# Kernel optimization log

Measured on AMD Instinct MI355X. Metric: run time of the kernel, lower is better.

The kernel has to match this reference:

```python
import math
import jax, jax.numpy as jnp
import numpy as np

B, N, H, K = 8, 1024, 200, 3
EDGE_SIZE = 50

def _layernorm(x, g, b, eps=1e-20):
    mu = jnp.mean(x, -1, keepdims=True)
    var = jnp.mean((x - mu) ** 2, -1, keepdims=True)
    return (x - mu) / jnp.sqrt(var + eps) * g + b

def _bert_layer(x, mask_add, qw, qb, kw, kb, vw, vb, aow, aob, g1, b1, iw, ib, ow, ob, g2, b2):
    # single-head self-attention (num_heads=1 -> head_dim == H), eval mode (dropout = identity)
    q = x @ qw + qb
    k = x @ kw + kb
    v = x @ vw + vb
    scores = jnp.einsum('bnd,bmd->bnm', q, k) / math.sqrt(H) + mask_add  # [B,N,N]
    probs = jax.nn.softmax(scores, -1)
    ctx = jnp.einsum('bnm,bmd->bnd', probs, v)
    attn = _layernorm(ctx @ aow + aob + x, g1, b1)
    inter = jax.nn.gelu(attn @ iw + ib, approximate=False)
    return _layernorm(inter @ ow + ob + attn, g2, b2)

def setup_inputs():
    key = jax.random.key(0)
    ks = jax.random.split(key, 16)
    s = 0.02
    text = jax.random.normal(ks[0], (B, N, H), jnp.float32)
    adj1 = (jax.random.uniform(ks[1], (B, N, N)) < 0.02).astype(jnp.float32)
    adj1 = jnp.maximum(adj1, jnp.eye(N, dtype=jnp.float32))  # self loops
    adj2 = (jax.random.uniform(ks[2], (B, N, N)) < 0.02).astype(jnp.float32)
    edge1 = jax.random.randint(ks[3], (B, N, N), 0, EDGE_SIZE, jnp.int32)
    edge2 = jax.random.randint(ks[4], (B, N, N), 0, EDGE_SIZE, jnp.int32)
    lengths = jax.random.randint(ks[5], (B,), N // 2, N + 1)
    textmask = (jnp.arange(N)[None, :] < lengths[:, None]).astype(jnp.float32)
    def nrm(k, shape):
        return jax.random.normal(k, shape, jnp.float32) * s
    return dict(
        text=text, adj1=adj1, adj2=adj2, edge1=edge1, edge2=edge2, textmask=textmask,
        gcn_w=nrm(ks[6], (H, H)), mut_w=nrm(ks[7], (H, H)),
        qw=nrm(ks[8], (K, H, H)), qb=jnp.zeros((K, H), jnp.float32),
        kw=nrm(ks[9], (K, H, H)), kb=jnp.zeros((K, H), jnp.float32),
        vw=nrm(ks[10], (K, H, H)), vb=jnp.zeros((K, H), jnp.float32),
        aow=nrm(ks[11], (K, H, H)), aob=jnp.zeros((K, H), jnp.float32),
        ln1_g=jnp.ones((K, H), jnp.float32), ln1_b=jnp.zeros((K, H), jnp.float32),
        iw=nrm(ks[12], (K, H, H)), ib=jnp.zeros((K, H), jnp.float32),
        ow=nrm(ks[13], (K, H, H)), ob=jnp.zeros((K, H), jnp.float32),
        ln2_g=jnp.ones((K, H), jnp.float32), ln2_b=jnp.zeros((K, H), jnp.float32))

def reference(text, adj1, adj2, edge1, edge2, textmask, gcn_w, mut_w, qw, qb, kw, kb, vw, vb, aow, aob, ln1_g, ln1_b, iw, ib, ow, ob, ln2_g, ln2_b):
    # edge1/edge2 and edge_vocab are unused by the original forward
    adj = adj1 + adj2
    adj = jnp.where(adj >= 1.0, 1.0, adj)
    mask_add = ((1.0 - textmask) * -10000.0)[:, None, :]           # [B,1,N] key-side mask
    pair = textmask[:, :, None] * textmask[:, None, :]             # [B,N,N]
    pair_add = (1.0 - pair) * -10000.0
    denom = jnp.sum(adj, 2, keepdims=True) + 1e-07                 # [B,N,1]
    outs, output = text, text                                      # in_features == out_features path
    for i in range(K):
        outs = _bert_layer(outs, mask_add, qw[i], qb[i], kw[i], kb[i], vw[i], vb[i],
                           aow[i], aob[i], ln1_g[i], ln1_b[i], iw[i], ib[i], ow[i], ob[i], ln2_g[i], ln2_b[i])
        # GCN propagation: adj-matmul -> degree normalize -> relu -> residual (dropout = identity in eval)
        teout = output @ gcn_w
        output = jax.nn.relu(jnp.einsum('bnm,bmd->bnd', adj, teout) / denom) + output
        # selfalignment: dual masked softmax attention between outs and output
        logit = jnp.einsum('bnd,bmd->bnm', outs @ mut_w, output) + pair_add
        p_row = jax.nn.softmax(logit, -1)
        p_col = jax.nn.softmax(logit, -2)
        new_outs = jnp.einsum('bnm,bmd->bnd', p_row, output) * textmask[:, :, None] + outs
        output = jnp.einsum('bnm,bnd->bmd', p_col, outs) * textmask[:, :, None] + output
        outs = new_outs
    return outs, adj
```

## Files before the change

### kernel.cpp

```cpp
#include <hip/hip_runtime.h>
#include <hip/hip_bf16.h>
#include <math.h>

#define Bd 8
#define Nd 1024
#define Hd 200
#define HP 224
#define BN (Bd*Nd)
#define SZ_BNH ((size_t)BN*Hd)
#define SZ_BNN ((size_t)BN*Nd)
#define SZ_PAD ((size_t)BN*HP)

typedef __hip_bfloat16 bf16;
typedef __attribute__((ext_vector_type(8))) short bf16x8;
typedef __attribute__((ext_vector_type(4))) float f32x4;

__device__ __forceinline__ float bf2f(bf16 v){ return __bfloat162float(v); }
__device__ __forceinline__ bf16 f2bf(float v){ return __float2bfloat16(v); }

#define MFMA16(a,b,c) __builtin_amdgcn_mfma_f32_16x16x32_bf16((a),(b),(c),0,0,0)

__device__ __forceinline__ size_t tidx1024(int row, int k){
  return (size_t)(row>>4)*16384 + (size_t)((k>>5))*512
       + (size_t)(((k>>3)&3))*128 + (size_t)(row&15)*8 + (k&7);
}
__device__ __forceinline__ size_t tidxHP(int row, int k){
  return (size_t)(row>>4)*3584 + (size_t)((k>>5))*512
       + (size_t)(((k>>3)&3))*128 + (size_t)(row&15)*8 + (k&7);
}

__global__ void k_prep_masks(const float* __restrict__ tm, float* __restrict__ maskf,
                             float* __restrict__ maskadd){
  int i = blockIdx.x*256 + threadIdx.x;
  if (i < BN){ float m = tm[i]; maskf[i] = m; maskadd[i] = (1.f - m) * -10000.f; }
}

__global__ void k_prep_adj(const float* __restrict__ a1, const float* __restrict__ a2,
                           float* __restrict__ adj_out, float* __restrict__ denom){
  int r = blockIdx.x;
  const size_t base = (size_t)r * Nd;
  int t = threadIdx.x;
  float s = 0.f;
  for (int m = t; m < Nd; m += 256){
    float a = a1[base+m] + a2[base+m];
    a = a >= 1.f ? 1.f : a;
    adj_out[base+m] = a;
    s += a;
  }
  __shared__ float red[256];
  red[t] = s; __syncthreads();
  for (int st = 128; st > 0; st >>= 1){ if (t < st) red[t] += red[t+st]; __syncthreads(); }
  if (t == 0) denom[r] = red[0] + 1e-07f;
}

__global__ void k_copy2(const float* __restrict__ x, float* __restrict__ o1,
                        float* __restrict__ o2){
  size_t i = (size_t)blockIdx.x*256 + threadIdx.x;
  if (i < SZ_BNH){ float v = x[i]; o1[i] = v; o2[i] = v; }
}

__global__ void c_pad_split(const float* __restrict__ X, bf16* __restrict__ Oh,
                            bf16* __restrict__ Ol){
  size_t o = (size_t)blockIdx.x*256 + threadIdx.x;
  if (o >= SZ_PAD) return;
  int oi = (int)o;
  int panel = oi / 3584;
  int rem   = oi % 3584;
  int kt  = rem >> 9;
  int kg  = (rem >> 7) & 3;
  int r16 = (rem >> 3) & 15;
  int ke  = rem & 7;
  int row = panel*16 + r16;
  int k   = kt*32 + kg*8 + ke;
  float v = (k < Hd) ? X[(size_t)row*Hd + k] : 0.f;
  bf16 h = f2bf(v);
  Oh[o] = h; Ol[o] = f2bf(v - bf2f(h));
}

__global__ void c_padT_split(const float* __restrict__ X, bf16* __restrict__ Oh,
                             bf16* __restrict__ Ol){
  __shared__ float t[32][33];
  int b = blockIdx.z, m0 = blockIdx.x*32, d0 = blockIdx.y*32;
  int tx = threadIdx.x, ty = threadIdx.y;
  for (int i = ty; i < 32; i += 8){
    int d = d0 + tx;
    t[i][tx] = (d < Hd) ? X[((size_t)b*Nd + m0+i)*Hd + d] : 0.f;
  }
  __syncthreads();
  for (int i = ty; i < 32; i += 8){
    int row = d0 + i, kk = m0 + tx;
    size_t idx = (size_t)b*229376 + tidx1024(row, kk);
    float v = t[tx][i];
    bf16 h = f2bf(v);
    Oh[idx] = h; Ol[idx] = f2bf(v - bf2f(h));
  }
}

__global__ void c_w_split_all(const float* __restrict__ g, const float* __restrict__ m,
                              const float* __restrict__ q, const float* __restrict__ k,
                              const float* __restrict__ v, const float* __restrict__ ao,
                              const float* __restrict__ iw, const float* __restrict__ ow,
                              bf16* __restrict__ Oh, bf16* __restrict__ Ol){
  int mi = blockIdx.y;
  const float* W;
  if (mi == 0) W = g;
  else if (mi == 1) W = m;
  else {
    int gi = (mi-2)/3, si = (mi-2)%3;
    const float* bs[6] = {q, k, v, ao, iw, ow};
    W = bs[gi] + (size_t)si*Hd*Hd;
  }
  int o = blockIdx.x*256 + threadIdx.x;
  if (o >= HP*HP) return;
  int panel = o / 3584;
  int rem   = o % 3584;
  int kt  = rem >> 9;
  int kg  = (rem >> 7) & 3;
  int r16 = (rem >> 3) & 15;
  int ke  = rem & 7;
  int n   = panel*16 + r16;
  int kk  = kt*32 + kg*8 + ke;
  float val = (n < Hd && kk < Hd) ? W[kk*Hd + n] : 0.f;
  bf16 h = f2bf(val);
  Oh[(size_t)mi*HP*HP + o] = h; Ol[(size_t)mi*HP*HP + o] = f2bf(val - bf2f(h));
}

__global__ void c_cvt1024_t(const float* __restrict__ X, bf16* __restrict__ O){
  int b = blockIdx.z, kg = blockIdx.x, rg = blockIdx.y;
  int r = threadIdx.x >> 5, kl = threadIdx.x & 31;
  int row = rg*8 + r, k = kg*32 + kl;
  float v = X[(size_t)b*1048576 + (size_t)row*1024 + k];
  O[(size_t)b*1048576 + tidx1024(row, k)] = f2bf(v);
}

__global__ void c_pcolT_split(const float* __restrict__ S, const float* __restrict__ cmax,
                              const float* __restrict__ csum, bf16* __restrict__ Ph,
                              bf16* __restrict__ Pl){
  __shared__ float t[32][33];
  int b = blockIdx.z, n0 = blockIdx.x*32, m0 = blockIdx.y*32;
  int tx = threadIdx.x, ty = threadIdx.y;
  for (int i = ty; i < 32; i += 8)
    t[i][tx] = S[(size_t)b*Nd*Nd + (size_t)(n0+i)*Nd + m0 + tx];
  __syncthreads();
  for (int i = ty; i < 32; i += 8){
    int m = m0 + i;
    float cm = cmax[b*Nd + m], ci = 1.f / csum[b*Nd + m];
    float p = expf(t[tx][i] - cm) * ci;
    size_t idx = (size_t)b*1048576 + tidx1024(m, n0 + tx);
    bf16 h = f2bf(p);
    Ph[idx] = h; Pl[idx] = f2bf(p - bf2f(h));
  }
}

template<int SPLIT>
__global__ __launch_bounds__(256)
void k_rowsoftmax(const float* __restrict__ S, bf16* __restrict__ Ph,
                  bf16* __restrict__ Pl){
  __shared__ float row[Nd];
  __shared__ float red[256];
  size_t bid = blockIdx.x;
  size_t r = ((bid & 7) << 10) + (bid >> 3);
  const float* src = S + r*Nd;
  int t = threadIdx.x;
  float mx = -3.4e38f;
  for (int i = t; i < Nd; i += 256){ float v = src[i]; row[i] = v; mx = fmaxf(mx, v); }
  red[t] = mx; __syncthreads();
  for (int s = 128; s > 0; s >>= 1){ if (t < s) red[t] = fmaxf(red[t], red[t+s]); __syncthreads(); }
  mx = red[0]; __syncthreads();
  float sum = 0.f;
  for (int i = t; i < Nd; i += 256) sum += expf(row[i] - mx);
  red[t] = sum; __syncthreads();
  for (int s = 128; s > 0; s >>= 1){ if (t < s) red[t] += red[t+s]; __syncthreads(); }
  float inv = 1.f / red[0];
  size_t obase = ((r >> 10) << 20) + (size_t)(((int)(r & 1023)) >> 4)*16384
               + (size_t)((int)r & 15)*8;
  for (int i = t; i < Nd; i += 256){
    float p = expf(row[i] - mx) * inv;
    bf16 h = f2bf(p);
    size_t idx = obase + (size_t)(i>>5)*512 + (size_t)((i>>3)&3)*128 + (i&7);
    Ph[idx] = h;
    if (SPLIT) Pl[idx] = f2bf(p - bf2f(h));
  }
}

__global__ __launch_bounds__(1024)
void k_colstats(const float* __restrict__ S, float* __restrict__ cmax,
                float* __restrict__ csum){
  int b = blockIdx.y;
  int tx = threadIdx.x & 63, ty = threadIdx.x >> 6;
  int m = blockIdx.x*64 + tx;
  const float* Sbp = S + (size_t)b*Nd*Nd + m;
  float mx = -3.4e38f, sm = 0.f;
  for (int n = ty; n < Nd; n += 16){
    float x = Sbp[(size_t)n*Nd];
    if (x > mx){ sm = sm * expf(mx - x) + 1.f; mx = x; }
    else        sm += expf(x - mx);
  }
  __shared__ float smx[16][64], ssm[16][64];
  smx[ty][tx] = mx; ssm[ty][tx] = sm;
  __syncthreads();
  for (int st = 8; st > 0; st >>= 1){
    if (ty < st){
      float m1 = smx[ty][tx],    s1 = ssm[ty][tx];
      float m2 = smx[ty+st][tx], s2 = ssm[ty+st][tx];
      float M = fmaxf(m1, m2);
      smx[ty][tx] = M;
      ssm[ty][tx] = s1*expf(m1 - M) + s2*expf(m2 - M);
    }
    __syncthreads();
  }
  if (ty == 0){ cmax[b*Nd + m] = smx[0][tx]; csum[b*Nd + m] = ssm[0][tx]; }
}

__global__ void k_add_ln(const float* __restrict__ X, const float* __restrict__ R,
                         const float* __restrict__ g, const float* __restrict__ bb,
                         float* __restrict__ Y, bf16* __restrict__ Ph,
                         bf16* __restrict__ Pl){
  int r = blockIdx.x, t = threadIdx.x;
  __shared__ float red[256];
  bool act = t < Hd;
  float v = 0.f;
  if (act) v = X[(size_t)r*Hd + t] + R[(size_t)r*Hd + t];
  red[t] = act ? v : 0.f; __syncthreads();
  for (int s = 128; s > 0; s >>= 1){ if (t < s) red[t] += red[t+s]; __syncthreads(); }
  float mu = red[0] * (1.f/Hd); __syncthreads();
  float d = act ? (v - mu) : 0.f;
  red[t] = d*d; __syncthreads();
  for (int s = 128; s > 0; s >>= 1){ if (t < s) red[t] += red[t+s]; __syncthreads(); }
  float var = red[0] * (1.f/Hd);
  float o = 0.f;
  if (act){
    float rs = 1.f / sqrtf(var + 1e-20f);
    o = (v - mu) * rs * g[t] + bb[t];
    Y[(size_t)r*Hd + t] = o;
  }
  if (Ph && t < HP){
    bf16 h = f2bf(o);
    size_t idx = tidxHP(r, t);
    Ph[idx] = h; Pl[idx] = f2bf(o - bf2f(h));
  }
}

template<int EPI, int TERMS, int RI, int KP>
__global__ __launch_bounds__(256)
void k_mfma3(const bf16* __restrict__ Ah, const bf16* __restrict__ Al,
             const bf16* __restrict__ Bh, const bf16* __restrict__ Bl,
             float* __restrict__ Y, bf16* __restrict__ Ybh, bf16* __restrict__ Ybl,
             const float* __restrict__ bias, const float* __restrict__ e0,
             const float* __restrict__ e1,
             size_t sAb, size_t sBb, float scale)
{
  int b = blockIdx.z;
  int wave = threadIdx.x >> 6, lane = threadIdx.x & 63;
  int r0 = (blockIdx.y*4 + wave)*(RI*16);
  int c0 = blockIdx.x*64;
  int lm = lane & 15, lq = lane >> 4;
  const size_t PST = (size_t)16*KP;
  const size_t aT = (size_t)b*sAb + (size_t)(r0>>4)*PST + (size_t)lane*8;
  const size_t bT = (size_t)b*sBb + (size_t)(c0>>4)*PST + (size_t)lane*8;
  constexpr int STEPS = KP/32;

  f32x4 acc[RI][4] = {};
  bf16x8 pah[2][RI], pal[2][RI], pbh[2][4], pbl[2][4];
  {
    #pragma unroll
    for (int i = 0; i < RI; i++) pah[0][i] = *(const bf16x8*)(Ah + aT + (size_t)i*PST);
    #pragma unroll
    for (int j = 0; j < 4; j++){
      pbh[0][j] = *(const bf16x8*)(Bh + bT + (size_t)j*PST);
      pbl[0][j] = *(const bf16x8*)(Bl + bT + (size_t)j*PST);
    }
    if (TERMS >= 3){
      #pragma unroll
      for (int i = 0; i < RI; i++) pal[0][i] = *(const bf16x8*)(Al + aT + (size_t)i*PST);
    }
  }

  #pragma unroll
  for (int ki = 0; ki < STEPS; ki++){
    const int cb = ki & 1, nb = cb ^ 1;
    if (ki + 1 < STEPS){
      const size_t kn = (size_t)(ki+1)*512;
      #pragma unroll
      for (int i = 0; i < RI; i++) pah[nb][i] = *(const bf16x8*)(Ah + aT + (size_t)i*PST + kn);
      #pragma unroll
      for (int j = 0; j < 4; j++){
        pbh[nb][j] = *(const bf16x8*)(Bh + bT + (size_t)j*PST + kn);
        pbl[nb][j] = *(const bf16x8*)(Bl + bT + (size_t)j*PST + kn);
      }
      if (TERMS >= 3){
        #pragma unroll
        for (int i = 0; i < RI; i++) pal[nb][i] = *(const bf16x8*)(Al + aT + (size_t)i*PST + kn);
      }
    }
    #pragma unroll
    for (int i = 0; i < RI; i++)
      #pragma unroll
      for (int j = 0; j < 4; j++) acc[i][j] = MFMA16(pah[cb][i], pbh[cb][j], acc[i][j]);
    #pragma unroll
    for (int i = 0; i < RI; i++)
      #pragma unroll
      for (int j = 0; j < 4; j++) acc[i][j] = MFMA16(pah[cb][i], pbl[cb][j], acc[i][j]);
    if (TERMS >= 3){
      #pragma unroll
      for (int i = 0; i < RI; i++)
        #pragma unroll
        for (int j = 0; j < 4; j++) acc[i][j] = MFMA16(pal[cb][i], pbh[cb][j], acc[i][j]);
    }
  }

  if constexpr (EPI == 9){
    __shared__ float tl[64][65];
    #pragma unroll
    for (int j = 0; j < 4; j++)
      #pragma unroll
      for (int r = 0; r < 4; r++)
        tl[wave*16 + lq*4 + r][j*16 + lm] = acc[0][j][r];
    __syncthreads();
    int b2 = (int)((blockIdx.y*64) >> 10);
    int m0 = (int)((blockIdx.y*64) & 1023);
    #pragma unroll
    for (int e = threadIdx.x; e < 4096; e += 256){
      int pan = e >> 10, rem = e & 1023;
      int r16 = (rem >> 3) & 15;
      int d = c0 + pan*16 + r16;
      if (d >= HP) continue;
      int kg = (rem >> 7) & 3;
      int k_loc = (rem >> 9)*32 + kg*8 + (rem & 7);
      float val = 0.f;
      if (d < Hd) val = tl[k_loc][pan*16 + r16] + (bias ? bias[d] : 0.f);
      bf16 h = f2bf(val);
      size_t idx = (size_t)b2*229376 + (size_t)(d>>4)*16384
                 + (size_t)((m0 + k_loc)>>5)*512 + (size_t)kg*128
                 + (size_t)r16*8 + (rem & 7);
      Ybh[idx] = h; Ybl[idx] = f2bf(val - bf2f(h));
    }
  } else {
    #pragma unroll
    for (int i = 0; i < RI; i++){
      #pragma unroll
      for (int j = 0; j < 4; j++){
        int col = c0 + j*16 + lm;
        int rbase = r0 + i*16 + lq*4;
        #pragma unroll
        for (int r = 0; r < 4; r++){
          int row = rbase + r;
          size_t rowg = (size_t)b*Nd + row;
          float v = acc[i][j][r];
          if (EPI == 0){
            if (col < Hd){
              v += bias ? bias[col] : 0.f;
              Y[rowg*Hd + col] = v;
            }
          } else if (EPI == 2){
            if (col < HP){
              float o = (col < Hd) ? v + (bias ? bias[col] : 0.f) : 0.f;
              bf16 h = f2bf(o);
              size_t idx = tidxHP((int)rowg, col);
              Ybh[idx] = h;
              Ybl[idx] = f2bf(o - bf2f(h));
            }
          } else if (EPI == 3){
            Y[rowg*Nd + col] = v*scale + e0[b*Nd + col];
          } else if (EPI == 4){
            Y[rowg*Nd + col] = v + (1.f - e1[b*Nd+row]*e1[b*Nd+col])*(-10000.f);
          } else if (EPI == 10){
            if (col < HP){
              float o = 0.f;
              if (col < Hd){
                float vv = v + (bias ? bias[col] : 0.f);
                o = 0.5f*vv*(1.f + erff(vv*0.7071067811865476f));
              }
              bf16 h = f2bf(o);
              size_t idx = tidxHP((int)rowg, col);
              Ybh[idx] = h;
              Ybl[idx] = f2bf(o - bf2f(h));
            }
          }
        }
      }
    }
  }
}

template<int EPI, int TERMS, int KP>
__global__ __launch_bounds__(256)
void k_mfma3sk(const bf16* __restrict__ Ah, const bf16* __restrict__ Al,
               const bf16* __restrict__ Bh, const bf16* __restrict__ Bl,
               float* __restrict__ Y, bf16* __restrict__ Ybh, bf16* __restrict__ Ybl,
               const float* __restrict__ e0, const float* __restrict__ e1,
               const float* __restrict__ R,
               size_t sAb, size_t sBb)
{
  __shared__ float red[4][64][33];
  int b = blockIdx.z;
  int wave = threadIdx.x >> 6, lane = threadIdx.x & 63;
  int r0 = blockIdx.x*32;
  int c0 = blockIdx.y*64;
  int lm = lane & 15, lq = lane >> 4;
  const size_t aT = (size_t)b*sAb + (size_t)(r0>>4)*((size_t)16*KP) + (size_t)lane*8;
  const size_t bT = (size_t)b*sBb + (size_t)(c0>>4)*((size_t)16*KP) + (size_t)lane*8;
  const int kt0 = wave*(KP>>7);
  constexpr int STEPS = KP/128;

  f32x4 acc[2][4] = {};
  bf16x8 pah[2][2], pal[2][2], pbh[2][4], pbl[2][4];
  {
    const size_t ko = (size_t)kt0*512;
    #pragma unroll
    for (int i = 0; i < 2; i++) pah[0][i] = *(const bf16x8*)(Ah + aT + (size_t)(i*16)*KP + ko);
    #pragma unroll
    for (int j = 0; j < 4; j++){
      pbh[0][j] = *(const bf16x8*)(Bh + bT + (size_t)(j*16)*KP + ko);
      pbl[0][j] = *(const bf16x8*)(Bl + bT + (size_t)(j*16)*KP + ko);
    }
    if (TERMS >= 3){
      #pragma unroll
      for (int i = 0; i < 2; i++) pal[0][i] = *(const bf16x8*)(Al + aT + (size_t)(i*16)*KP + ko);
    }
  }

  #pragma unroll
  for (int ki = 0; ki < STEPS; ki++){
    const int cb = ki & 1, nb = cb ^ 1;
    if (ki + 1 < STEPS){
      const size_t kn = (size_t)(kt0 + ki + 1)*512;
      #pragma unroll
      for (int i = 0; i < 2; i++) pah[nb][i] = *(const bf16x8*)(Ah + aT + (size_t)(i*16)*KP + kn);
      #pragma unroll
      for (int j = 0; j < 4; j++){
        pbh[nb][j] = *(const bf16x8*)(Bh + bT + (size_t)(j*16)*KP + kn);
        pbl[nb][j] = *(const bf16x8*)(Bl + bT + (size_t)(j*16)*KP + kn);
      }
      if (TERMS >= 3){
        #pragma unroll
        for (int i = 0; i < 2; i++) pal[nb][i] = *(const bf16x8*)(Al + aT + (size_t)(i*16)*KP + kn);
      }
    }
    #pragma unroll
    for (int i = 0; i < 2; i++)
      #pragma unroll
      for (int j = 0; j < 4; j++) acc[i][j] = MFMA16(pah[cb][i], pbh[cb][j], acc[i][j]);
    #pragma unroll
    for (int i = 0; i < 2; i++)
      #pragma unroll
      for (int j = 0; j < 4; j++) acc[i][j] = MFMA16(pah[cb][i], pbl[cb][j], acc[i][j]);
    if (TERMS >= 3){
      #pragma unroll
      for (int i = 0; i < 2; i++)
        #pragma unroll
        for (int j = 0; j < 4; j++) acc[i][j] = MFMA16(pal[cb][i], pbh[cb][j], acc[i][j]);
    }
  }

  #pragma unroll
  for (int i = 0; i < 2; i++)
    #pragma unroll
    for (int j = 0; j < 4; j++)
      #pragma unroll
      for (int r = 0; r < 4; r++)
        red[wave][lane][i*16 + j*4 + r] = acc[i][j][r];
  __syncthreads();

  int iw = wave >> 1, j0 = (wave & 1)*2;
  #pragma unroll
  for (int jj = 0; jj < 2; jj++){
    int j = j0 + jj;
    int col = c0 + j*16 + lm;
    #pragma unroll
    for (int r = 0; r < 4; r++){
      int f = iw*16 + j*4 + r;
      float v = red[0][lane][f] + red[1][lane][f] + red[2][lane][f] + red[3][lane][f];
      int row = r0 + iw*16 + lq*4 + r;
      size_t rowg = (size_t)b*Nd + row;
      if (col < HP){
        float nv = 0.f;
        if (EPI == 8){
          nv = (col < Hd) ? v : 0.f;
        } else if (EPI == 5){
          if (col < Hd){
            float u = v / e0[b*Nd+row]; u = u > 0.f ? u : 0.f;
            nv = Y[rowg*Hd + col] + u;
            Y[rowg*Hd + col] = nv;
          }
        } else if (EPI == 6){
          if (col < Hd){
            nv = v*e1[b*Nd+row] + R[rowg*Hd+col];
            Y[rowg*Hd + col] = nv;
          }
        } else if (EPI == 7){
          if (col < Hd){
            nv = v*e1[b*Nd+row] + Y[rowg*Hd+col];
            Y[rowg*Hd + col] = nv;
          }
        }
        bf16 h = f2bf(nv);
        size_t idx = tidxHP((int)rowg, col);
        Ybh[idx] = h; Ybl[idx] = f2bf(nv - bf2f(h));
      }
    }
  }
}

static inline char* carve(char*& p, size_t bytes){
  char* r = p;
  p += (bytes + 511) & ~(size_t)511;
  return r;
}

extern "C" void kernel_launch(void* const* d_in, const int* in_sizes, int n_in,
                              void* d_out, int out_size, void* d_ws, size_t ws_size,
                              hipStream_t stream){
  (void)in_sizes; (void)n_in; (void)out_size; (void)ws_size;
  const float* text     = (const float*)d_in[0];
  const float* adj1     = (const float*)d_in[1];
  const float* adj2     = (const float*)d_in[2];
  const float* textmask = (const float*)d_in[5];
  const float* gcn_w    = (const float*)d_in[6];
  const float* mut_w    = (const float*)d_in[7];
  const float* qw = (const float*)d_in[8],  *qb = (const float*)d_in[9];
  const float* kw = (const float*)d_in[10], *kb = (const float*)d_in[11];
  const float* vw = (const float*)d_in[12], *vb = (const float*)d_in[13];
  const float* aow= (const float*)d_in[14], *aob= (const float*)d_in[15];
  const float* g1 = (const float*)d_in[16], *b1 = (const float*)d_in[17];
  const float* iw = (const float*)d_in[18], *ib = (const float*)d_in[19];
  const float* ow = (const float*)d_in[20], *ob = (const float*)d_in[21];
  const float* g2 = (const float*)d_in[22], *b2 = (const float*)d_in[23];

  float* out_outs = (float*)d_out;
  float* out_adj  = out_outs + SZ_BNH;

  char* p = (char*)d_ws;
  float* cur  = (float*)carve(p, SZ_BNH*4);
  float* sc1  = (float*)carve(p, SZ_BNH*4);
  float* fo   = (float*)carve(p, SZ_BNH*4);
  float* S    = (float*)carve(p, SZ_BNN*4);
  bf16*  Rb   = (bf16*)carve(p, SZ_BNN*2*2);
  bf16*  T1   = (bf16*)carve(p, SZ_PAD*2);
  bf16*  T2   = (bf16*)carve(p, SZ_PAD*2);
  bf16*  T3   = (bf16*)carve(p, SZ_PAD*2);
  bf16*  T4   = (bf16*)carve(p, SZ_PAD*2);
  bf16*  T5   = (bf16*)carve(p, SZ_PAD*2);
  bf16*  T6   = (bf16*)carve(p, SZ_PAD*2);
  bf16*  TA1  = (bf16*)carve(p, SZ_PAD*2);
  bf16*  TA2  = (bf16*)carve(p, SZ_PAD*2);
  bf16*  TF1  = (bf16*)carve(p, SZ_PAD*2);
  bf16*  TF2  = (bf16*)carve(p, SZ_PAD*2);
  bf16*  ADJB = (bf16*)carve(p, SZ_BNN*2);
  bf16*  Wh_all = (bf16*)carve(p, (size_t)21*HP*HP*2);
  bf16*  Wl_all = (bf16*)carve(p, (size_t)21*HP*HP*2);
  float* denom   = (float*)carve(p, BN*4);
  float* maskf   = (float*)carve(p, BN*4);
  float* maskadd = (float*)carve(p, BN*4);
  float* cmaxv   = (float*)carve(p, BN*4);
  float* csumv   = (float*)carve(p, BN*4);

  float* sc2 = out_outs;
  bf16* attnP = Rb;
  bf16* Ph    = Rb;
  bf16* Pl    = Rb + SZ_BNN;

  const size_t sNT = (size_t)Nd*HP;
  const size_t sT  = (size_t)HP*Nd;
  const size_t sNN = (size_t)Nd*Nd;

  #define W_GCN 0
  #define W_MUT 1
  #define W_Q(i) (2 + (i))
  #define W_K(i) (5 + (i))
  #define W_V(i) (8 + (i))
  #define W_AO(i) (11 + (i))
  #define W_IW(i) (14 + (i))
  #define W_OW(i) (17 + (i))
  #define WH(s) (Wh_all + (size_t)(s)*HP*HP)
  #define WL(s) (Wl_all + (size_t)(s)*HP*HP)

  dim3 blk256(256);
  dim3 gPad((unsigned)((SZ_PAD+255)/256));
  dim3 gPadT(32, 7, Bd), bT(32, 8);
  dim3 gPcolT(32, 32, Bd);
  dim3 gWall((HP*HP+255)/256, 20);
  dim3 gCvt(32, 128, Bd);
  dim3 gBNH((unsigned)((SZ_BNH+255)/256));
  dim3 gSm(4, 128, 1);
  dim3 gNT(16, 8, Bd);
  dim3 gSK(32, 4, Bd);
  const float inv_sqrt_h = 0.07071067811865475f;
  const size_t Z = 0;

  k_prep_masks<<<(BN+255)/256, blk256, 0, stream>>>(textmask, maskf, maskadd);
  k_prep_adj<<<BN, blk256, 0, stream>>>(adj1, adj2, out_adj, denom);
  k_copy2<<<gBNH, blk256, 0, stream>>>(text, cur, fo);
  c_w_split_all<<<gWall, blk256, 0, stream>>>(gcn_w, mut_w, qw, kw, vw, aow, iw, ow,
                                              Wh_all, Wl_all);
  c_pad_split<<<gPad, blk256, 0, stream>>>(cur, TA1, TA2);
  c_pad_split<<<gPad, blk256, 0, stream>>>(fo,  TF1, TF2);
  c_cvt1024_t<<<gCvt, blk256, 0, stream>>>(out_adj, ADJB);

  for (int i = 0; i < 3; i++){
    const float *qbi = qb + i*Hd;
    const float *kbi = kb + i*Hd;
    const float *vbi = vb + i*Hd;
    const float *aobi= aob+ i*Hd;
    const float *g1i = g1 + i*Hd,    *b1i = b1 + i*Hd;
    const float *ibi = ib + i*Hd;
    const float *obi = ob + i*Hd;
    const float *g2i = g2 + i*Hd,    *b2i = b2 + i*Hd;

    k_mfma3<2,3,1,HP><<<gSm, blk256, 0, stream>>>(TA1,TA2,WH(W_Q(i)),WL(W_Q(i)),
              nullptr,T3,T4, qbi, nullptr,nullptr, Z,Z, 0.f);
    k_mfma3<2,3,1,HP><<<gSm, blk256, 0, stream>>>(TA1,TA2,WH(W_K(i)),WL(W_K(i)),
              nullptr,T5,T6, kbi, nullptr,nullptr, Z,Z, 0.f);
    k_mfma3<3,3,2,HP><<<gNT, blk256, 0, stream>>>(T3,T4,T5,T6, S,nullptr,nullptr,
              nullptr, maskadd,nullptr, sNT,sNT, inv_sqrt_h);
    k_mfma3<9,3,1,HP><<<gSm, blk256, 0, stream>>>(TA1,TA2,WH(W_V(i)),WL(W_V(i)),
              nullptr,T1,T2, vbi, nullptr,nullptr, Z,Z, 0.f);
    k_rowsoftmax<0><<<BN, blk256, 0, stream>>>(S, attnP, nullptr);
    k_mfma3sk<8,2,Nd><<<gSK, blk256, 0, stream>>>(attnP,nullptr,T1,T2,
              nullptr,T3,T4, nullptr,nullptr,nullptr, sNN,sT);
    k_mfma3<0,3,1,HP><<<gSm, blk256, 0, stream>>>(T3,T4,WH(W_AO(i)),WL(W_AO(i)),
              sc1,nullptr,nullptr, aobi, nullptr,nullptr, Z,Z, 0.f);
    k_add_ln<<<BN, blk256, 0, stream>>>(sc1, cur, g1i, b1i, sc2, T1, T2);
    k_mfma3<10,3,1,HP><<<gSm, blk256, 0, stream>>>(T1,T2,WH(W_IW(i)),WL(W_IW(i)),
              nullptr,T3,T4, ibi, nullptr,nullptr, Z,Z, 0.f);
    k_mfma3<0,3,1,HP><<<gSm, blk256, 0, stream>>>(T3,T4,WH(W_OW(i)),WL(W_OW(i)),
              cur,nullptr,nullptr, obi, nullptr,nullptr, Z,Z, 0.f);
    k_add_ln<<<BN, blk256, 0, stream>>>(cur, sc2, g2i, b2i, cur, TA1, TA2);

    k_mfma3<9,3,1,HP><<<gSm, blk256, 0, stream>>>(TF1,TF2,WH(W_GCN),WL(W_GCN),
              nullptr,T1,T2, nullptr, nullptr,nullptr, Z,Z, 0.f);
    k_mfma3sk<5,2,Nd><<<gSK, blk256, 0, stream>>>(ADJB,nullptr,T1,T2,
              fo,TF1,TF2, denom,nullptr,nullptr, sNN,sT);

    k_mfma3<2,3,1,HP><<<gSm, blk256, 0, stream>>>(TA1,TA2,WH(W_MUT),WL(W_MUT),
              nullptr,T5,T6, nullptr, nullptr,nullptr, Z,Z, 0.f);
    k_mfma3<4,3,2,HP><<<gNT, blk256, 0, stream>>>(T5,T6,TF1,TF2, S,nullptr,nullptr,
              nullptr, nullptr,maskf, sNT,sNT, 0.f);
    k_colstats<<<dim3(Nd/64, Bd), dim3(1024), 0, stream>>>(S, cmaxv, csumv);
    k_rowsoftmax<1><<<BN, blk256, 0, stream>>>(S, Ph, Pl);
    c_padT_split<<<gPadT, bT, 0, stream>>>(fo, T1, T2);
    k_mfma3sk<6,3,Nd><<<gSK, blk256, 0, stream>>>(Ph,Pl,T1,T2,
              (i==2)?out_outs:sc1, TA1,TA2, nullptr,maskf,cur, sNN,sT);
    c_pcolT_split<<<gPcolT, bT, 0, stream>>>(S, cmaxv, csumv, Ph, Pl);
    c_padT_split<<<gPadT, bT, 0, stream>>>(cur, T3, T4);
    k_mfma3sk<7,3,Nd><<<gSK, blk256, 0, stream>>>(Ph,Pl,T3,T4,
              fo,TF1,TF2, nullptr,maskf,nullptr, sNN,sT);

    float* t = cur; cur = sc1; sc1 = t;
  }
}
```

Measured before the change: 1.301 ms.

## Fuse QKV projections, fold column softmax stats into GEMM epilogue, emit transposed tiles

Merges the Q/K/V projection GEMMs into one launch and moves the column max/sum computation into the masked-logit GEMM epilogue as per-block partials, which a small combine kernel then reduces. The row-softmax kernel now also writes the column-softmax probabilities, so the separate strided column-stats pass and the transpose kernel go away. The GCN kernel additionally writes a transposed bf16 copy of the output, which removes one padT conversion. Also reorders the two alignment GEMMs and uses the raw input for the initial padding. These changes cut launches and the full N×N re-reads, at the cost of extra buffers and scattered transposed stores.

```diff
diff --git a/kernel.cpp b/kernel.cpp
--- a/kernel.cpp
+++ b/kernel.cpp
@@ -133,29 +133,12 @@
   O[(size_t)b*1048576 + tidx1024(row, k)] = f2bf(v);
 }
 
-__global__ void c_pcolT_split(const float* __restrict__ S, const float* __restrict__ cmax,
-                              const float* __restrict__ csum, bf16* __restrict__ Ph,
-                              bf16* __restrict__ Pl){
-  __shared__ float t[32][33];
-  int b = blockIdx.z, n0 = blockIdx.x*32, m0 = blockIdx.y*32;
-  int tx = threadIdx.x, ty = threadIdx.y;
-  for (int i = ty; i < 32; i += 8)
-    t[i][tx] = S[(size_t)b*Nd*Nd + (size_t)(n0+i)*Nd + m0 + tx];
-  __syncthreads();
-  for (int i = ty; i < 32; i += 8){
-    int m = m0 + i;
-    float cm = cmax[b*Nd + m], ci = 1.f / csum[b*Nd + m];
-    float p = expf(t[tx][i] - cm) * ci;
-    size_t idx = (size_t)b*1048576 + tidx1024(m, n0 + tx);
-    bf16 h = f2bf(p);
-    Ph[idx] = h; Pl[idx] = f2bf(p - bf2f(h));
-  }
-}
-
 template<int SPLIT>
 __global__ __launch_bounds__(256)
 void k_rowsoftmax(const float* __restrict__ S, bf16* __restrict__ Ph,
-                  bf16* __restrict__ Pl){
+                  bf16* __restrict__ Pl, const float* __restrict__ cmax,
+                  const float* __restrict__ csum, bf16* __restrict__ PcH,
+                  bf16* __restrict__ PcL){
   __shared__ float row[Nd];
   __shared__ float red[256];
   size_t bid = blockIdx.x;
@@ -179,37 +162,34 @@
     bf16 h = f2bf(p);
     size_t idx = obase + (size_t)(i>>5)*512 + (size_t)((i>>3)&3)*128 + (i&7);
     Ph[idx] = h;
-    if (SPLIT) Pl[idx] = f2bf(p - bf2f(h));
-  }
-}
-
-__global__ __launch_bounds__(1024)
-void k_colstats(const float* __restrict__ S, float* __restrict__ cmax,
-                float* __restrict__ csum){
-  int b = blockIdx.y;
-  int tx = threadIdx.x & 63, ty = threadIdx.x >> 6;
-  int m = blockIdx.x*64 + tx;
-  const float* Sbp = S + (size_t)b*Nd*Nd + m;
-  float mx = -3.4e38f, sm = 0.f;
-  for (int n = ty; n < Nd; n += 16){
-    float x = Sbp[(size_t)n*Nd];
-    if (x > mx){ sm = sm * expf(mx - x) + 1.f; mx = x; }
-    else        sm += expf(x - mx);
-  }
-  __shared__ float smx[16][64], ssm[16][64];
-  smx[ty][tx] = mx; ssm[ty][tx] = sm;
-  __syncthreads();
-  for (int st = 8; st > 0; st >>= 1){
-    if (ty < st){
-      float m1 = smx[ty][tx],    s1 = ssm[ty][tx];
-      float m2 = smx[ty+st][tx], s2 = ssm[ty+st][tx];
-      float M = fmaxf(m1, m2);
-      smx[ty][tx] = M;
-      ssm[ty][tx] = s1*expf(m1 - M) + s2*expf(m2 - M);
-    }
-    __syncthreads();
-  }
-  if (ty == 0){ cmax[b*Nd + m] = smx[0][tx]; csum[b*Nd + m] = ssm[0][tx]; }
+    if (SPLIT == 2) Pl[idx] = f2bf(p - bf2f(h));
+  }
+  if (SPLIT == 2){
+    int bq = (int)(r >> 10);
+    int n  = (int)(r & 1023);
+    size_t nb = (size_t)bq * 1048576;
+    for (int m = t; m < Nd; m += 256){
+      float ci = 1.f / csum[bq*Nd + m];
+      float p = expf(row[m] - cmax[bq*Nd + m]) * ci;
+      bf16 h = f2bf(p);
+      size_t idx = nb + tidx1024(m, n);
+      PcH[idx] = h; PcL[idx] = f2bf(p - bf2f(h));
+    }
+  }
+}
+
+__global__ void k_colcomb(const float* __restrict__ cpm, const float* __restrict__ cps,
+                          float* __restrict__ cmax, float* __restrict__ csum){
+  int i = blockIdx.x*256 + threadIdx.x;
+  float M = cpm[i], S = cps[i];
+  #pragma unroll
+  for (int y = 1; y < 8; y++){
+    float m2 = cpm[(size_t)y*BN + i], s2 = cps[(size_t)y*BN + i];
+    float Mn = fmaxf(M, m2);
+    S = S*expf(M - Mn) + s2*expf(m2 - Mn);
+    M = Mn;
+  }
+  cmax[i] = M; csum[i] = S;
 }
 
 __global__ void k_add_ln(const float* __restrict__ X, const float* __restrict__ R,
@@ -241,6 +221,102 @@
   }
 }
 
+__global__ __launch_bounds__(256)
+void k_qkv(const bf16* __restrict__ Ah, const bf16* __restrict__ Al,
+           const bf16* __restrict__ Wh0, const bf16* __restrict__ Wl0,
+           bf16* __restrict__ QH, bf16* __restrict__ QL,
+           bf16* __restrict__ KH, bf16* __restrict__ KL,
+           bf16* __restrict__ VH, bf16* __restrict__ VL,
+           const float* __restrict__ qb, const float* __restrict__ kb,
+           const float* __restrict__ vb)
+{
+  constexpr int KP = HP;
+  constexpr int STEPS = KP/32;
+  int slice = blockIdx.z;
+  int wave = threadIdx.x >> 6, lane = threadIdx.x & 63;
+  int r0 = (blockIdx.y*4 + wave)*16;
+  int c0 = blockIdx.x*64;
+  int lm = lane & 15, lq = lane >> 4;
+  const size_t PST = (size_t)16*KP;
+  const size_t aT = (size_t)(r0>>4)*PST + (size_t)lane*8;
+  const size_t bT = (size_t)slice*3*HP*HP + (size_t)(c0>>4)*PST + (size_t)lane*8;
+
+  f32x4 acc[4] = {};
+  bf16x8 pah[2], pal[2], pbh[2][4], pbl[2][4];
+  pah[0] = *(const bf16x8*)(Ah + aT);
+  pal[0] = *(const bf16x8*)(Al + aT);
+  #pragma unroll
+  for (int j = 0; j < 4; j++){
+    pbh[0][j] = *(const bf16x8*)(Wh0 + bT + (size_t)j*PST);
+    pbl[0][j] = *(const bf16x8*)(Wl0 + bT + (size_t)j*PST);
+  }
+  #pragma unroll
+  for (int ki = 0; ki < STEPS; ki++){
+    const int cb = ki & 1, nb = cb ^ 1;
+    if (ki + 1 < STEPS){
+      const size_t kn = (size_t)(ki+1)*512;
+      pah[nb] = *(const bf16x8*)(Ah + aT + kn);
+      pal[nb] = *(const bf16x8*)(Al + aT + kn);
+      #pragma unroll
+      for (int j = 0; j < 4; j++){
+        pbh[nb][j] = *(const bf16x8*)(Wh0 + bT + (size_t)j*PST + kn);
+        pbl[nb][j] = *(const bf16x8*)(Wl0 + bT + (size_t)j*PST + kn);
+      }
+    }
+    #pragma unroll
+    for (int j = 0; j < 4; j++) acc[j] = MFMA16(pah[cb], pbh[cb][j], acc[j]);
+    #pragma unroll
+    for (int j = 0; j < 4; j++) acc[j] = MFMA16(pah[cb], pbl[cb][j], acc[j]);
+    #pragma unroll
+    for (int j = 0; j < 4; j++) acc[j] = MFMA16(pal[cb], pbh[cb][j], acc[j]);
+  }
+
+  const float* bias = (slice == 0) ? qb : (slice == 1) ? kb : vb;
+  if (slice < 2){
+    bf16* Oh = (slice == 0) ? QH : KH;
+    bf16* Ol = (slice == 0) ? QL : KL;
+    #pragma unroll
+    for (int j = 0; j < 4; j++){
+      int col = c0 + j*16 + lm;
+      if (col >= HP) continue;
+      #pragma unroll
+      for (int r = 0; r < 4; r++){
+        int row = r0 + lq*4 + r;
+        float o = (col < Hd) ? acc[j][r] + bias[col] : 0.f;
+        bf16 h = f2bf(o);
+        size_t idx = tidxHP(row, col);
+        Oh[idx] = h; Ol[idx] = f2bf(o - bf2f(h));
+      }
+    }
+  } else {
+    __shared__ float tl[64][65];
+    #pragma unroll
+    for (int j = 0; j < 4; j++)
+      #pragma unroll
+      for (int r = 0; r < 4; r++)
+        tl[wave*16 + lq*4 + r][j*16 + lm] = acc[j][r];
+    __syncthreads();
+    int b2 = (int)((blockIdx.y*64) >> 10);
+    int m0 = (int)((blockIdx.y*64) & 1023);
+    #pragma unroll
+    for (int e = threadIdx.x; e < 4096; e += 256){
+      int pan = e >> 10, rem = e & 1023;
+      int r16 = (rem >> 3) & 15;
+      int d = c0 + pan*16 + r16;
+      if (d >= HP) continue;
+      int kg = (rem >> 7) & 3;
+      int k_loc = (rem >> 9)*32 + kg*8 + (rem & 7);
+      float val = 0.f;
+      if (d < Hd) val = tl[k_loc][pan*16 + r16] + bias[d];
+      bf16 h = f2bf(val);
+      size_t idx = (size_t)b2*229376 + (size_t)(d>>4)*16384
+                 + (size_t)((m0 + k_loc)>>5)*512 + (size_t)kg*128
+                 + (size_t)r16*8 + (rem & 7);
+      VH[idx] = h; VL[idx] = f2bf(val - bf2f(h));
+    }
+  }
+}
+
 template<int EPI, int TERMS, int RI, int KP>
 __global__ __launch_bounds__(256)
 void k_mfma3(const bf16* __restrict__ Ah, const bf16* __restrict__ Al,
@@ -248,7 +324,8 @@
              float* __restrict__ Y, bf16* __restrict__ Ybh, bf16* __restrict__ Ybl,
              const float* __restrict__ bias, const float* __restrict__ e0,
              const float* __restrict__ e1,
-             size_t sAb, size_t sBb, float scale)
+             size_t sAb, size_t sBb, float scale,
+             float* __restrict__ cpm, float* __restrict__ cps)
 {
   int b = blockIdx.z;
   int wave = threadIdx.x >> 6, lane = threadIdx.x & 63;
@@ -334,6 +411,70 @@
                  + (size_t)((m0 + k_loc)>>5)*512 + (size_t)kg*128
                  + (size_t)r16*8 + (rem & 7);
       Ybh[idx] = h; Ybl[idx] = f2bf(val - bf2f(h));
+    }
+  } else if constexpr (EPI == 4){
+    float er[RI][4];
+    #pragma unroll
+    for (int i = 0; i < RI; i++)
+      #pragma unroll
+      for (int r = 0; r < 4; r++)
+        er[i][r] = e1[b*Nd + r0 + i*16 + lq*4 + r];
+    float cm[4], cs[4];
+    #pragma unroll
+    for (int j = 0; j < 4; j++){
+      int col = c0 + j*16 + lm;
+      float e1c = e1[b*Nd + col];
+      float wv[RI][4];
+      float mloc = -3.4e38f;
+      #pragma unroll
+      for (int i = 0; i < RI; i++){
+        #pragma unroll
+        for (int r = 0; r < 4; r++){
+          int row = r0 + i*16 + lq*4 + r;
+          float w = acc[i][j][r] + (1.f - er[i][r]*e1c)*(-10000.f);
+          Y[((size_t)b*Nd + row)*Nd + col] = w;
+          wv[i][r] = w;
+          mloc = fmaxf(mloc, w);
+        }
+      }
+      float sloc = 0.f;
+      #pragma unroll
+      for (int i = 0; i < RI; i++)
+        #pragma unroll
+        for (int r = 0; r < 4; r++) sloc += expf(wv[i][r] - mloc);
+      cm[j] = mloc; cs[j] = sloc;
+    }
+    #pragma unroll
+    for (int j = 0; j < 4; j++){
+      float m = cm[j], s = cs[j];
+      #pragma unroll
+      for (int off = 16; off <= 32; off <<= 1){
+        float m2 = __shfl_xor(m, off), s2 = __shfl_xor(s, off);
+        float M = fmaxf(m, m2);
+        s = s*expf(m - M) + s2*expf(m2 - M);
+        m = M;
+      }
+      cm[j] = m; cs[j] = s;
+    }
+    __shared__ float pmx[4][4][16], psm[4][4][16];
+    if (lq == 0){
+      #pragma unroll
+      for (int j = 0; j < 4; j++){ pmx[wave][j][lm] = cm[j]; psm[wave][j][lm] = cs[j]; }
+    }
+    __syncthreads();
+    if (threadIdx.x < 64){
+      int t = threadIdx.x;
+      int jj = t >> 4, cc = t & 15;
+      float M = pmx[0][jj][cc], S = psm[0][jj][cc];
+      #pragma unroll
+      for (int w = 1; w < 4; w++){
+        float m2 = pmx[w][jj][cc], s2 = psm[w][jj][cc];
+        float Mn = fmaxf(M, m2);
+        S = S*expf(M - Mn) + s2*expf(m2 - Mn);
+        M = Mn;
+      }
+      size_t pi = (size_t)blockIdx.y*BN + (size_t)b*Nd + c0 + t;
+      cpm[pi] = M; cps[pi] = S;
     }
   } else {
     #pragma unroll
@@ -362,8 +503,6 @@
             }
           } else if (EPI == 3){
             Y[rowg*Nd + col] = v*scale + e0[b*Nd + col];
-          } else if (EPI == 4){
-            Y[rowg*Nd + col] = v + (1.f - e1[b*Nd+row]*e1[b*Nd+col])*(-10000.f);
           } else if (EPI == 10){
             if (col < HP){
               float o = 0.f;
@@ -390,7 +529,8 @@
                float* __restrict__ Y, bf16* __restrict__ Ybh, bf16* __restrict__ Ybl,
                const float* __restrict__ e0, const float* __restrict__ e1,
                const float* __restrict__ R,
-               size_t sAb, size_t sBb)
+               size_t sAb, size_t sBb,
+               bf16* __restrict__ TbH, bf16* __restrict__ TbL)
 {
   __shared__ float red[4][64][33];
   int b = blockIdx.z;
@@ -495,8 +635,13 @@
           }
         }
         bf16 h = f2bf(nv);
+        bf16 lo = f2bf(nv - bf2f(h));
         size_t idx = tidxHP((int)rowg, col);
-        Ybh[idx] = h; Ybl[idx] = f2bf(nv - bf2f(h));
+        Ybh[idx] = h; Ybl[idx] = lo;
+        if (TbH != nullptr){
+          size_t idx2 = (size_t)b*((size_t)HP*Nd) + tidx1024(col, row);
+          TbH[idx2] = h; TbL[idx2] = lo;
+        }
       }
     }
   }
@@ -536,6 +681,7 @@
   float* fo   = (float*)carve(p, SZ_BNH*4);
   float* S    = (float*)carve(p, SZ_BNN*4);
   bf16*  Rb   = (bf16*)carve(p, SZ_BNN*2*2);
+  bf16*  Rc   = (bf16*)carve(p, SZ_BNN*2*2);
   bf16*  T1   = (bf16*)carve(p, SZ_PAD*2);
   bf16*  T2   = (bf16*)carve(p, SZ_PAD*2);
   bf16*  T3   = (bf16*)carve(p, SZ_PAD*2);
@@ -546,9 +692,13 @@
   bf16*  TA2  = (bf16*)carve(p, SZ_PAD*2);
   bf16*  TF1  = (bf16*)carve(p, SZ_PAD*2);
   bf16*  TF2  = (bf16*)carve(p, SZ_PAD*2);
+  bf16*  TT1  = (bf16*)carve(p, SZ_PAD*2);
+  bf16*  TT2  = (bf16*)carve(p, SZ_PAD*2);
   bf16*  ADJB = (bf16*)carve(p, SZ_BNN*2);
   bf16*  Wh_all = (bf16*)carve(p, (size_t)21*HP*HP*2);
   bf16*  Wl_all = (bf16*)carve(p, (size_t)21*HP*HP*2);
+  float* cpm     = (float*)carve(p, (size_t)8*BN*4);
+  float* cps     = (float*)carve(p, (size_t)8*BN*4);
   float* denom   = (float*)carve(p, BN*4);
   float* maskf   = (float*)carve(p, BN*4);
   float* maskadd = (float*)carve(p, BN*4);
@@ -559,6 +709,8 @@
   bf16* attnP = Rb;
   bf16* Ph    = Rb;
   bf16* Pl    = Rb + SZ_BNN;
+  bf16* PcH   = Rc;
+  bf16* PcL   = Rc + SZ_BNN;
 
   const size_t sNT = (size_t)Nd*HP;
   const size_t sT  = (size_t)HP*Nd;
@@ -578,23 +730,25 @@
   dim3 blk256(256);
   dim3 gPad((unsigned)((SZ_PAD+255)/256));
   dim3 gPadT(32, 7, Bd), bT(32, 8);
-  dim3 gPcolT(32, 32, Bd);
   dim3 gWall((HP*HP+255)/256, 20);
   dim3 gCvt(32, 128, Bd);
   dim3 gBNH((unsigned)((SZ_BNH+255)/256));
   dim3 gSm(4, 128, 1);
+  dim3 gQKV(4, 128, 3);
   dim3 gNT(16, 8, Bd);
   dim3 gSK(32, 4, Bd);
   const float inv_sqrt_h = 0.07071067811865475f;
   const size_t Z = 0;
+  float* FN = nullptr;
+  bf16*  BN_ = nullptr;
 
   k_prep_masks<<<(BN+255)/256, blk256, 0, stream>>>(textmask, maskf, maskadd);
   k_prep_adj<<<BN, blk256, 0, stream>>>(adj1, adj2, out_adj, denom);
   k_copy2<<<gBNH, blk256, 0, stream>>>(text, cur, fo);
   c_w_split_all<<<gWall, blk256, 0, stream>>>(gcn_w, mut_w, qw, kw, vw, aow, iw, ow,
                                               Wh_all, Wl_all);
-  c_pad_split<<<gPad, blk256, 0, stream>>>(cur, TA1, TA2);
-  c_pad_split<<<gPad, blk256, 0, stream>>>(fo,  TF1, TF2);
+  c_pad_split<<<gPad, blk256, 0, stream>>>(text, TA1, TA2);
+  c_pad_split<<<gPad, blk256, 0, stream>>>(text, TF1, TF2);
   c_cvt1024_t<<<gCvt, blk256, 0, stream>>>(out_adj, ADJB);
 
   for (int i = 0; i < 3; i++){
@@ -607,44 +761,38 @@
     const float *obi = ob + i*Hd;
     const float *g2i = g2 + i*Hd,    *b2i = b2 + i*Hd;
 
-    k_mfma3<2,3,1,HP><<<gSm, blk256, 0, stream>>>(TA1,TA2,WH(W_Q(i)),WL(W_Q(i)),
-              nullptr,T3,T4, qbi, nullptr,nullptr, Z,Z, 0.f);
-    k_mfma3<2,3,1,HP><<<gSm, blk256, 0, stream>>>(TA1,TA2,WH(W_K(i)),WL(W_K(i)),
-              nullptr,T5,T6, kbi, nullptr,nullptr, Z,Z, 0.f);
-    k_mfma3<3,3,2,HP><<<gNT, blk256, 0, stream>>>(T3,T4,T5,T6, S,nullptr,nullptr,
-              nullptr, maskadd,nullptr, sNT,sNT, inv_sqrt_h);
-    k_mfma3<9,3,1,HP><<<gSm, blk256, 0, stream>>>(TA1,TA2,WH(W_V(i)),WL(W_V(i)),
-              nullptr,T1,T2, vbi, nullptr,nullptr, Z,Z, 0.f);
-    k_rowsoftmax<0><<<BN, blk256, 0, stream>>>(S, attnP, nullptr);
-    k_mfma3sk<8,2,Nd><<<gSK, blk256, 0, stream>>>(attnP,nullptr,T1,T2,
-              nullptr,T3,T4, nullptr,nullptr,nullptr, sNN,sT);
+    k_qkv<<<gQKV, blk256, 0, stream>>>(TA1,TA2, WH(W_Q(i)),WL(W_Q(i)),
+              T3,T4, T5,T6, T1,T2, qbi,kbi,vbi);
+    k_mfma3<3,3,2,HP><<<gNT, blk256, 0, stream>>>(T3,T4,T5,T6, S,BN_,BN_,
+              nullptr, maskadd,nullptr, sNT,sNT, inv_sqrt_h, FN,FN);
+    k_rowsoftmax<0><<<BN, blk256, 0, stream>>>(S, attnP, BN_, FN,FN, BN_,BN_);
+    k_mfma3sk<8,2,Nd><<<gSK, blk256, 0, stream>>>(attnP,BN_,T1,T2,
+              FN,T3,T4, FN,FN,FN, sNN,sT, BN_,BN_);
     k_mfma3<0,3,1,HP><<<gSm, blk256, 0, stream>>>(T3,T4,WH(W_AO(i)),WL(W_AO(i)),
-              sc1,nullptr,nullptr, aobi, nullptr,nullptr, Z,Z, 0.f);
+              sc1,BN_,BN_, aobi, FN,FN, Z,Z, 0.f, FN,FN);
     k_add_ln<<<BN, blk256, 0, stream>>>(sc1, cur, g1i, b1i, sc2, T1, T2);
     k_mfma3<10,3,1,HP><<<gSm, blk256, 0, stream>>>(T1,T2,WH(W_IW(i)),WL(W_IW(i)),
-              nullptr,T3,T4, ibi, nullptr,nullptr, Z,Z, 0.f);
+              FN,T3,T4, ibi, FN,FN, Z,Z, 0.f, FN,FN);
     k_mfma3<0,3,1,HP><<<gSm, blk256, 0, stream>>>(T3,T4,WH(W_OW(i)),WL(W_OW(i)),
-              cur,nullptr,nullptr, obi, nullptr,nullptr, Z,Z, 0.f);
+              cur,BN_,BN_, obi, FN,FN, Z,Z, 0.f, FN,FN);
     k_add_ln<<<BN, blk256, 0, stream>>>(cur, sc2, g2i, b2i, cur, TA1, TA2);
 
     k_mfma3<9,3,1,HP><<<gSm, blk256, 0, stream>>>(TF1,TF2,WH(W_GCN),WL(W_GCN),
-              nullptr,T1,T2, nullptr, nullptr,nullptr, Z,Z, 0.f);
-    k_mfma3sk<5,2,Nd><<<gSK, blk256, 0, stream>>>(ADJB,nullptr,T1,T2,
-              fo,TF1,TF2, denom,nullptr,nullptr, sNN,sT);
+              FN,T1,T2, nullptr, FN,FN, Z,Z, 0.f, FN,FN);
+    k_mfma3sk<5,2,Nd><<<gSK, blk256, 0, stream>>>(ADJB,BN_,T1,T2,
+              fo,TF1,TF2, denom,FN,FN, sNN,sT, TT1,TT2);
 
     k_mfma3<2,3,1,HP><<<gSm, blk256, 0, stream>>>(TA1,TA2,WH(W_MUT),WL(W_MUT),
-              nullptr,T5,T6, nullptr, nullptr,nullptr, Z,Z, 0.f);
-    k_mfma3<4,3,2,HP><<<gNT, blk256, 0, stream>>>(T5,T6,TF1,TF2, S,nullptr,nullptr,
-              nullptr, nullptr,maskf, sNT,sNT, 0.f);
-    k_colstats<<<dim3(Nd/64, Bd), dim3(1024), 0, stream>>>(S, cmaxv, csumv);
-    k_rowsoftmax<1><<<BN, blk256, 0, stream>>>(S, Ph, Pl);
-    c_padT_split<<<gPadT, bT, 0, stream>>>(fo, T1, T2);
-    k_mfma3sk<6,3,Nd><<<gSK, blk256, 0, stream>>>(Ph,Pl,T1,T2,
-              (i==2)?out_outs:sc1, TA1,TA2, nullptr,maskf,cur, sNN,sT);
-    c_pcolT_split<<<gPcolT, bT, 0, stream>>>(S, cmaxv, csumv, Ph, Pl);
+              FN,T5,T6, nullptr, FN,FN, Z,Z, 0.f, FN,FN);
+    k_mfma3<4,3,2,HP><<<gNT, blk256, 0, stream>>>(T5,T6,TF1,TF2, S,BN_,BN_,
+              nullptr, nullptr,maskf, sNT,sNT, 0.f, cpm,cps);
+    k_colcomb<<<BN/256, blk256, 0, stream>>>(cpm, cps, cmaxv, csumv);
+    k_rowsoftmax<2><<<BN, blk256, 0, stream>>>(S, Ph, Pl, cmaxv, csumv, PcH, PcL);
     c_padT_split<<<gPadT, bT, 0, stream>>>(cur, T3, T4);
-    k_mfma3sk<7,3,Nd><<<gSK, blk256, 0, stream>>>(Ph,Pl,T3,T4,
-              fo,TF1,TF2, nullptr,maskf,nullptr, sNN,sT);
+    k_mfma3sk<6,3,Nd><<<gSK, blk256, 0, stream>>>(Ph,Pl,TT1,TT2,
+              (i==2)?out_outs:sc1, TA1,TA2, FN,maskf,cur, sNN,sT, BN_,BN_);
+    k_mfma3sk<7,3,Nd><<<gSK, blk256, 0, stream>>>(PcH,PcL,T3,T4,
+              fo,TF1,TF2, FN,maskf,FN, sNN,sT, BN_,BN_);
 
     float* t = cur; cur = sc1; sc1 = t;
   }
```

Result: faster. 1.186 ms (-8.9%).
